# Performance work log

Hardware: AMD Instinct MI355X
Metric: run time of the kernel (lower is better)

Reference implementation:

```python
import jax, jax.numpy as jnp
import numpy as np

N = 20000      # nodes
E = 320000     # edges (before self-loops)
D = 128        # esm_embeds
H = 4          # n_heads (layer 1)
G = 256        # graphs in batch
SLOPE = 0.2    # GATConv default negative_slope


def setup_inputs() -> dict:
    key = jax.random.key(0)
    ks = jax.random.split(key, 16)
    x = jax.random.normal(ks[0], (N, D), jnp.float32)
    src = jax.random.randint(ks[1], (E,), 0, N)
    off = jax.random.randint(ks[2], (E,), 1, N)
    dst = (src + off) % N  # guaranteed no self-loops (PyG removes then re-adds them)
    edge_index = jnp.stack([src, dst]).astype(jnp.int64)
    batch = jnp.sort(jax.random.randint(ks[3], (N,), 0, G)).astype(jnp.int64)
    s = 0.05
    W1 = jax.random.normal(ks[4], (D, H * D), jnp.float32) * s
    a_src1 = jax.random.normal(ks[5], (1, H, D), jnp.float32) * s
    a_dst1 = jax.random.normal(ks[6], (1, H, D), jnp.float32) * s
    b1 = jnp.zeros((H * D,), jnp.float32)
    W2 = jax.random.normal(ks[7], (H * D, D), jnp.float32) * s
    a_src2 = jax.random.normal(ks[8], (1, 1, D), jnp.float32) * s
    a_dst2 = jax.random.normal(ks[9], (1, 1, D), jnp.float32) * s
    b2 = jnp.zeros((D,), jnp.float32)
    fc1_w = jax.random.normal(ks[10], (D, 16), jnp.float32) * s
    fc1_b = jnp.zeros((16,), jnp.float32)
    fc2_w = jax.random.normal(ks[11], (16, 1), jnp.float32) * s
    fc2_b = jnp.zeros((1,), jnp.float32)
    return {"x": x, "edge_index": edge_index, "batch": batch,
            "W1": W1, "a_src1": a_src1, "a_dst1": a_dst1, "b1": b1,
            "W2": W2, "a_src2": a_src2, "a_dst2": a_dst2, "b2": b2,
            "fc1_w": fc1_w, "fc1_b": fc1_b, "fc2_w": fc2_w, "fc2_b": fc2_b}


def _gat_conv(h, src, dst, a_src, a_dst, n):
    """h: [n, heads, C]; returns aggregated [n, heads, C] (PyG GATConv message passing)."""
    al_s = jnp.sum(h * a_src, axis=-1)  # [n, heads]
    al_d = jnp.sum(h * a_dst, axis=-1)  # [n, heads]
    e = jax.nn.leaky_relu(al_s[src] + al_d[dst], SLOPE)  # [Etot, heads]
    m = jax.lax.stop_gradient(jax.ops.segment_max(e, dst, num_segments=n))
    ex = jnp.exp(e - m[dst])
    denom = jax.ops.segment_sum(ex, dst, num_segments=n)
    alpha = ex / denom[dst]                               # per-destination softmax
    msg = h[src] * alpha[..., None]                       # [Etot, heads, C]
    return jax.ops.segment_sum(msg, dst, num_segments=n)


def reference(x, edge_index, batch, W1, a_src1, a_dst1, b1,
              W2, a_src2, a_dst2, b2, fc1_w, fc1_b, fc2_w, fc2_b):
    n = x.shape[0]
    loop = jnp.arange(n, dtype=edge_index.dtype)
    src = jnp.concatenate([edge_index[0], loop])  # GATConv add_self_loops=True
    dst = jnp.concatenate([edge_index[1], loop])
    # layer 1: heads=H, concat -> [n, H*D], then ELU (dropout is identity in eval)
    h1 = (x @ W1).reshape(n, H, D)
    o1 = _gat_conv(h1, src, dst, a_src1, a_dst1, n).reshape(n, H * D) + b1
    x1 = jax.nn.elu(o1)
    # layer 2: heads=1, concat -> [n, D], then ReLU
    h2 = (x1 @ W2).reshape(n, 1, D)
    o2 = _gat_conv(h2, src, dst, a_src2, a_dst2, n).reshape(n, D) + b2
    x2 = jax.nn.relu(o2)
    # global max pool over graphs; x2 >= 0 so clamping handles any empty segment
    pooled = jnp.maximum(jax.ops.segment_max(x2, batch, num_segments=G), 0.0)
    hfc = jax.nn.relu(pooled @ fc1_w + fc1_b)
    return hfc @ fc2_w + fc2_b  # [G, 1]
```

## Files before the change

kernel.cpp:

```cpp
#include <hip/hip_runtime.h>
#include <hip/hip_fp16.h>

#define N_NODES 20000
#define E_EDGES 320000
#define D_DIM   128
#define H1HEADS 4
#define G_GRAPHS 256
#define SLOPE   0.2f

typedef short short8 __attribute__((ext_vector_type(8)));
typedef float float4v __attribute__((ext_vector_type(4)));

__global__ void cnt_k(const int* __restrict__ dst, int* __restrict__ cnt) {
    int e = blockIdx.x * blockDim.x + threadIdx.x;
    if (e < E_EDGES) atomicAdd(&cnt[dst[e]], 1);
}

__global__ __launch_bounds__(256) void scan_k(const int* __restrict__ cnt,
                                              int* __restrict__ rowptr) {
    __shared__ int s[256];
    const int t = threadIdx.x;
    const int CH = (N_NODES + 255) / 256;
    int base = t * CH;
    int sum = 0;
    for (int i = 0; i < CH; ++i) {
        int idx = base + i;
        if (idx < N_NODES) sum += cnt[idx];
    }
    s[t] = sum;
    __syncthreads();
    for (int off = 1; off < 256; off <<= 1) {
        int v = (t >= off) ? s[t - off] : 0;
        __syncthreads();
        s[t] += v;
        __syncthreads();
    }
    int run = (t > 0) ? s[t - 1] : 0;
    for (int i = 0; i < CH; ++i) {
        int idx = base + i;
        if (idx < N_NODES) { rowptr[idx] = run; run += cnt[idx]; }
    }
    if (t == 255) rowptr[N_NODES] = run;
}

__global__ void scat_k(const int* __restrict__ src, const int* __restrict__ dst,
                       const int* __restrict__ rowptr, int* __restrict__ cur,
                       int* __restrict__ csrsrc) {
    int e = blockIdx.x * blockDim.x + threadIdx.x;
    if (e >= E_EDGES) return;
    int d = dst[e];
    int p = rowptr[d] + atomicAdd(&cur[d], 1);
    csrsrc[p] = src[e];
}

__device__ __forceinline__ unsigned short f2bf(float f) {
    unsigned u = __float_as_uint(f);
    unsigned r = u + 0x7FFFu + ((u >> 16) & 1u);
    return (unsigned short)(r >> 16);
}
__device__ __forceinline__ float bf2f(unsigned short b) {
    return __uint_as_float((unsigned)b << 16);
}

__global__ void split_k(const float* __restrict__ in, unsigned short* __restrict__ hi,
                        unsigned short* __restrict__ lo, const int n) {
    int i = blockIdx.x * blockDim.x + threadIdx.x;
    if (i >= n) return;
    float v = in[i];
    unsigned short h = f2bf(v);
    hi[i] = h;
    lo[i] = f2bf(v - bf2f(h));
}

__global__ void splitT_k(const float* __restrict__ w, unsigned short* __restrict__ hiT,
                         unsigned short* __restrict__ loT, const int K, const int N) {
    int i = blockIdx.x * blockDim.x + threadIdx.x;
    if (i >= K * N) return;
    int k = i / N, n = i - k * N;
    float v = w[i];
    unsigned short h = f2bf(v);
    hiT[n * K + k] = h;
    loT[n * K + k] = f2bf(v - bf2f(h));
}

__device__ __forceinline__ void store_val(__half* p, float v) { *p = __float2half(v); }
__device__ __forceinline__ void store_val(float* p, float v) { *p = v; }

template <typename OT>
__global__ __launch_bounds__(256) void mgemm_k(const unsigned short* __restrict__ Ahi,
                                               const unsigned short* __restrict__ Alo,
                                               const unsigned short* __restrict__ BThi,
                                               const unsigned short* __restrict__ BTlo,
                                               const int M, const int N, const int K,
                                               OT* __restrict__ C) {
    constexpr int SA = 72;
    __shared__ unsigned short Ah[64 * SA], Al[64 * SA];
    __shared__ unsigned short Bh[128 * SA], Bl[128 * SA];
    const int t = threadIdx.x;
    const int wave = t >> 6, lane = t & 63;
    const int q = lane >> 4, rr = lane & 15;
    const int row0 = blockIdx.x * 64;
    const int col0 = blockIdx.y * 128;
    const int wm = wave & 1, wn = wave >> 1;

    float4v acc[2][4];
#pragma unroll
    for (int i = 0; i < 2; ++i)
#pragma unroll
        for (int j = 0; j < 4; ++j) acc[i][j] = (float4v){0.f, 0.f, 0.f, 0.f};

    for (int kc = 0; kc < K; kc += 64) {
        __syncthreads();
#pragma unroll
        for (int i = 0; i < 2; ++i) {
            int u = t + i * 256;
            int m = u >> 3, mac = u & 7;
            int r = row0 + m;
            uint4 vh = {0, 0, 0, 0}, vl = {0, 0, 0, 0};
            if (r < M) {
                vh = *(const uint4*)(Ahi + (size_t)r * K + kc + mac * 8);
                vl = *(const uint4*)(Alo + (size_t)r * K + kc + mac * 8);
            }
            *(uint4*)(Ah + m * SA + mac * 8) = vh;
            *(uint4*)(Al + m * SA + mac * 8) = vl;
        }
#pragma unroll
        for (int i = 0; i < 4; ++i) {
            int u = t + i * 256;
            int n = u >> 3, mac = u & 7;
            *(uint4*)(Bh + n * SA + mac * 8) =
                *(const uint4*)(BThi + (size_t)(col0 + n) * K + kc + mac * 8);
            *(uint4*)(Bl + n * SA + mac * 8) =
                *(const uint4*)(BTlo + (size_t)(col0 + n) * K + kc + mac * 8);
        }
        __syncthreads();
#pragma unroll
        for (int ks = 0; ks < 2; ++ks) {
            const int ko = ks * 32 + q * 8;
            short8 ah[2], alo[2], bh[4], blo[4];
#pragma unroll
            for (int mt = 0; mt < 2; ++mt) {
                int m = (wm * 2 + mt) * 16 + rr;
                ah[mt]  = *(const short8*)(Ah + m * SA + ko);
                alo[mt] = *(const short8*)(Al + m * SA + ko);
            }
#pragma unroll
            for (int nt = 0; nt < 4; ++nt) {
                int n = (wn * 4 + nt) * 16 + rr;
                bh[nt]  = *(const short8*)(Bh + n * SA + ko);
                blo[nt] = *(const short8*)(Bl + n * SA + ko);
            }
#pragma unroll
            for (int mt = 0; mt < 2; ++mt)
#pragma unroll
                for (int nt = 0; nt < 4; ++nt) {
                    acc[mt][nt] = __builtin_amdgcn_mfma_f32_16x16x32_bf16(
                        ah[mt], bh[nt], acc[mt][nt], 0, 0, 0);
                    acc[mt][nt] = __builtin_amdgcn_mfma_f32_16x16x32_bf16(
                        ah[mt], blo[nt], acc[mt][nt], 0, 0, 0);
                    acc[mt][nt] = __builtin_amdgcn_mfma_f32_16x16x32_bf16(
                        alo[mt], bh[nt], acc[mt][nt], 0, 0, 0);
                }
        }
    }
#pragma unroll
    for (int mt = 0; mt < 2; ++mt) {
#pragma unroll
        for (int reg = 0; reg < 4; ++reg) {
            int r = row0 + (wm * 2 + mt) * 16 + q * 4 + reg;
            if (r < M) {
#pragma unroll
                for (int nt = 0; nt < 4; ++nt) {
                    int c = col0 + (wn * 4 + nt) * 16 + rr;
                    store_val(&C[(size_t)r * N + c], acc[mt][nt][reg]);
                }
            }
        }
    }
}

__device__ __forceinline__ int bitonic64(int key, int lane) {
#pragma unroll
    for (int k = 2; k <= 64; k <<= 1) {
#pragma unroll
        for (int j = k >> 1; j > 0; j >>= 1) {
            int other = __shfl_xor(key, j);
            bool up = ((lane & k) == 0);
            bool lower = ((lane & j) == 0);
            int mn = min(key, other), mx = max(key, other);
            key = (up == lower) ? mn : mx;
        }
    }
    return key;
}

__global__ __launch_bounds__(256) void al16_k(const __half* __restrict__ h,
                                              const float* __restrict__ a_src,
                                              const float* __restrict__ a_dst,
                                              float* __restrict__ als,
                                              float* __restrict__ ald,
                                              const int NH, const int H) {
    int wid = (blockIdx.x * blockDim.x + threadIdx.x) >> 6;
    int lane = threadIdx.x & 63;
    if (wid >= NH) return;
    int hh = wid % H;
    const __half2* row = (const __half2*)(h + (size_t)wid * 128);
    float2 v = __half22float2(row[lane]);
    float2 as2 = ((const float2*)(a_src + hh * 128))[lane];
    float2 ad2 = ((const float2*)(a_dst + hh * 128))[lane];
    float s = v.x * as2.x + v.y * as2.y;
    float d = v.x * ad2.x + v.y * ad2.y;
#pragma unroll
    for (int off = 32; off > 0; off >>= 1) {
        s += __shfl_down(s, off);
        d += __shfl_down(d, off);
    }
    if (lane == 0) { als[wid] = s; ald[wid] = d; }
}

__global__ __launch_bounds__(256) void al32_k(const float* __restrict__ h,
                                              const float* __restrict__ a_src,
                                              const float* __restrict__ a_dst,
                                              float* __restrict__ als,
                                              float* __restrict__ ald,
                                              const int NH) {
    int wid = (blockIdx.x * blockDim.x + threadIdx.x) >> 6;
    int lane = threadIdx.x & 63;
    if (wid >= NH) return;
    float2 v = ((const float2*)(h + (size_t)wid * 128))[lane];
    float2 as2 = ((const float2*)a_src)[lane];
    float2 ad2 = ((const float2*)a_dst)[lane];
    float s = v.x * as2.x + v.y * as2.y;
    float d = v.x * ad2.x + v.y * ad2.y;
#pragma unroll
    for (int off = 32; off > 0; off >>= 1) {
        s += __shfl_down(s, off);
        d += __shfl_down(d, off);
    }
    if (lane == 0) { als[wid] = s; ald[wid] = d; }
}

__device__ __forceinline__ float lrelu(float v) { return (v > 0.f) ? v : SLOPE * v; }

__global__ __launch_bounds__(256) void agg1_k(const __half* __restrict__ h,
                                              const float4* __restrict__ als4,
                                              const float4* __restrict__ ald4,
                                              const int* __restrict__ rowptr,
                                              const int* __restrict__ csrsrc,
                                              const float* __restrict__ bias,
                                              unsigned short* __restrict__ x1hi,
                                              unsigned short* __restrict__ x1lo) {
    const int node = (blockIdx.x * blockDim.x + threadIdx.x) >> 6;
    if (node >= N_NODES) return;
    const int lane = threadIdx.x & 63;
    const int head = lane >> 4;
    const int r0 = rowptr[node];
    const int deg = rowptr[node + 1] - r0;
    const int tot = deg + 1;
    const float4 aldn = ald4[node];

    float acc[8] = {};
    float4 d4;

    if (tot <= 64) {
        int key = 0x7FFFFFFF;
        if (lane < deg) key = csrsrc[r0 + lane];
        else if (lane == deg) key = node;
        key = bitonic64(key, lane);
        int s = (lane < tot) ? key : node;
        float4 l4 = make_float4(-1e30f, -1e30f, -1e30f, -1e30f);
        if (lane < tot) {
            float4 a = als4[s];
            l4.x = lrelu(a.x + aldn.x); l4.y = lrelu(a.y + aldn.y);
            l4.z = lrelu(a.z + aldn.z); l4.w = lrelu(a.w + aldn.w);
        }
        float4 m4 = l4;
#pragma unroll
        for (int off = 32; off > 0; off >>= 1) {
            m4.x = fmaxf(m4.x, __shfl_xor(m4.x, off));
            m4.y = fmaxf(m4.y, __shfl_xor(m4.y, off));
            m4.z = fmaxf(m4.z, __shfl_xor(m4.z, off));
            m4.w = fmaxf(m4.w, __shfl_xor(m4.w, off));
        }
        float4 w4 = make_float4(0.f, 0.f, 0.f, 0.f);
        if (lane < tot) {
            w4.x = expf(l4.x - m4.x); w4.y = expf(l4.y - m4.y);
            w4.z = expf(l4.z - m4.z); w4.w = expf(l4.w - m4.w);
        }
        d4 = w4;
#pragma unroll
        for (int off = 32; off > 0; off >>= 1) {
            d4.x += __shfl_xor(d4.x, off);
            d4.y += __shfl_xor(d4.y, off);
            d4.z += __shfl_xor(d4.z, off);
            d4.w += __shfl_xor(d4.w, off);
        }
        for (int j = 0; j < tot; ++j) {
            int sj = __shfl(s, j);
            float w0 = __shfl(w4.x, j), w1 = __shfl(w4.y, j);
            float w2 = __shfl(w4.z, j), w3 = __shfl(w4.w, j);
            float wj = (head < 2) ? (head == 0 ? w0 : w1) : (head == 2 ? w2 : w3);
            const uint4 pk = *((const uint4*)(h + (size_t)sj * 512) + lane);
            const __half2* p2 = (const __half2*)&pk;
            float2 f0 = __half22float2(p2[0]);
            float2 f1 = __half22float2(p2[1]);
            float2 f2 = __half22float2(p2[2]);
            float2 f3 = __half22float2(p2[3]);
            acc[0] += wj * f0.x; acc[1] += wj * f0.y;
            acc[2] += wj * f1.x; acc[3] += wj * f1.y;
            acc[4] += wj * f2.x; acc[5] += wj * f2.y;
            acc[6] += wj * f3.x; acc[7] += wj * f3.y;
        }
    } else {
        float4 m4 = make_float4(-1e30f, -1e30f, -1e30f, -1e30f);
        for (int base = 0; base < tot; base += 64) {
            int j = base + lane;
            float4 l4 = make_float4(-1e30f, -1e30f, -1e30f, -1e30f);
            if (j < tot) {
                int s = (j < deg) ? csrsrc[r0 + j] : node;
                float4 a = als4[s];
                l4.x = lrelu(a.x + aldn.x); l4.y = lrelu(a.y + aldn.y);
                l4.z = lrelu(a.z + aldn.z); l4.w = lrelu(a.w + aldn.w);
            }
#pragma unroll
            for (int off = 32; off > 0; off >>= 1) {
                l4.x = fmaxf(l4.x, __shfl_xor(l4.x, off));
                l4.y = fmaxf(l4.y, __shfl_xor(l4.y, off));
                l4.z = fmaxf(l4.z, __shfl_xor(l4.z, off));
                l4.w = fmaxf(l4.w, __shfl_xor(l4.w, off));
            }
            m4.x = fmaxf(m4.x, l4.x); m4.y = fmaxf(m4.y, l4.y);
            m4.z = fmaxf(m4.z, l4.z); m4.w = fmaxf(m4.w, l4.w);
        }
        d4 = make_float4(0.f, 0.f, 0.f, 0.f);
        for (int base = 0; base < tot; base += 64) {
            int j = base + lane;
            int s = node;
            float4 w4 = make_float4(0.f, 0.f, 0.f, 0.f);
            if (j < tot) {
                if (j < deg) s = csrsrc[r0 + j];
                float4 a = als4[s];
                w4.x = expf(lrelu(a.x + aldn.x) - m4.x);
                w4.y = expf(lrelu(a.y + aldn.y) - m4.y);
                w4.z = expf(lrelu(a.z + aldn.z) - m4.z);
                w4.w = expf(lrelu(a.w + aldn.w) - m4.w);
            }
            float4 p4 = w4;
#pragma unroll
            for (int off = 32; off > 0; off >>= 1) {
                p4.x += __shfl_xor(p4.x, off);
                p4.y += __shfl_xor(p4.y, off);
                p4.z += __shfl_xor(p4.z, off);
                p4.w += __shfl_xor(p4.w, off);
            }
            d4.x += p4.x; d4.y += p4.y; d4.z += p4.z; d4.w += p4.w;
            int lim = min(64, tot - base);
            for (int j2 = 0; j2 < lim; ++j2) {
                int sj = __shfl(s, j2);
                float w0 = __shfl(w4.x, j2), w1 = __shfl(w4.y, j2);
                float w2 = __shfl(w4.z, j2), w3 = __shfl(w4.w, j2);
                float wj = (head < 2) ? (head == 0 ? w0 : w1) : (head == 2 ? w2 : w3);
                const uint4 pk = *((const uint4*)(h + (size_t)sj * 512) + lane);
                const __half2* p2 = (const __half2*)&pk;
                float2 f0 = __half22float2(p2[0]);
                float2 f1 = __half22float2(p2[1]);
                float2 f2 = __half22float2(p2[2]);
                float2 f3 = __half22float2(p2[3]);
                acc[0] += wj * f0.x; acc[1] += wj * f0.y;
                acc[2] += wj * f1.x; acc[3] += wj * f1.y;
                acc[4] += wj * f2.x; acc[5] += wj * f2.y;
                acc[6] += wj * f3.x; acc[7] += wj * f3.y;
            }
        }
    }

    const float dsel = (head < 2) ? (head == 0 ? d4.x : d4.y) : (head == 2 ? d4.z : d4.w);
    const float inv = 1.f / dsel;
    const float4 b0 = ((const float4*)bias)[lane * 2];
    const float4 b1 = ((const float4*)bias)[lane * 2 + 1];
    float v[8];
    v[0] = acc[0] * inv + b0.x; v[1] = acc[1] * inv + b0.y;
    v[2] = acc[2] * inv + b0.z; v[3] = acc[3] * inv + b0.w;
    v[4] = acc[4] * inv + b1.x; v[5] = acc[5] * inv + b1.y;
    v[6] = acc[6] * inv + b1.z; v[7] = acc[7] * inv + b1.w;
    uint4 ph, pl;
    unsigned short* hps = (unsigned short*)&ph;
    unsigned short* lps = (unsigned short*)&pl;
#pragma unroll
    for (int k = 0; k < 8; ++k) {
        float e = (v[k] > 0.f) ? v[k] : expm1f(v[k]);
        unsigned short hb = f2bf(e);
        hps[k] = hb;
        lps[k] = f2bf(e - bf2f(hb));
    }
    *(uint4*)(x1hi + (size_t)node * 512 + lane * 8) = ph;
    *(uint4*)(x1lo + (size_t)node * 512 + lane * 8) = pl;
}

__global__ __launch_bounds__(256) void agg2_k(const float* __restrict__ h,
                                              const float* __restrict__ als,
                                              const float* __restrict__ ald,
                                              const int* __restrict__ rowptr,
                                              const int* __restrict__ csrsrc,
                                              const float* __restrict__ bias,
                                              const int* __restrict__ batch,
                                              int* __restrict__ pooled) {
    const int node = (blockIdx.x * blockDim.x + threadIdx.x) >> 6;
    if (node >= N_NODES) return;
    const int lane = threadIdx.x & 63;
    const int r0 = rowptr[node];
    const int deg = rowptr[node + 1] - r0;
    const int tot = deg + 1;
    const float aldn = ald[node];

    float acc0 = 0.f, acc1 = 0.f;
    float denom;

    if (tot <= 64) {
        int key = 0x7FFFFFFF;
        if (lane < deg) key = csrsrc[r0 + lane];
        else if (lane == deg) key = node;
        key = bitonic64(key, lane);
        int s = (lane < tot) ? key : node;
        float l = -1e30f, w = 0.f;
        if (lane < tot) l = lrelu(als[s] + aldn);
        float m = l;
#pragma unroll
        for (int off = 32; off > 0; off >>= 1) m = fmaxf(m, __shfl_xor(m, off));
        if (lane < tot) w = expf(l - m);
        denom = w;
#pragma unroll
        for (int off = 32; off > 0; off >>= 1) denom += __shfl_xor(denom, off);
        for (int j = 0; j < tot; ++j) {
            int sj = __shfl(s, j);
            float wj = __shfl(w, j);
            float2 f = ((const float2*)(h + (size_t)sj * 128))[lane];
            acc0 += wj * f.x;
            acc1 += wj * f.y;
        }
    } else {
        float m = -1e30f;
        for (int base = 0; base < tot; base += 64) {
            int j = base + lane;
            float l = -1e30f;
            if (j < tot) {
                int s = (j < deg) ? csrsrc[r0 + j] : node;
                l = lrelu(als[s] + aldn);
            }
#pragma unroll
            for (int off = 32; off > 0; off >>= 1) l = fmaxf(l, __shfl_xor(l, off));
            m = fmaxf(m, l);
        }
        denom = 0.f;
        for (int base = 0; base < tot; base += 64) {
            int j = base + lane;
            int s = node;
            float w = 0.f;
            if (j < tot) {
                if (j < deg) s = csrsrc[r0 + j];
                w = expf(lrelu(als[s] + aldn) - m);
            }
            float ws = w;
#pragma unroll
            for (int off = 32; off > 0; off >>= 1) ws += __shfl_xor(ws, off);
            denom += ws;
            int lim = min(64, tot - base);
            for (int j2 = 0; j2 < lim; ++j2) {
                int sj = __shfl(s, j2);
                float wj = __shfl(w, j2);
                float2 f = ((const float2*)(h + (size_t)sj * 128))[lane];
                acc0 += wj * f.x;
                acc1 += wj * f.y;
            }
        }
    }

    const float inv = 1.f / denom;
    float v0 = fmaxf(acc0 * inv + bias[lane * 2], 0.f);
    float v1 = fmaxf(acc1 * inv + bias[lane * 2 + 1], 0.f);
    int* pb = pooled + batch[node] * 128;
    atomicMax(&pb[lane * 2], __float_as_int(v0));
    atomicMax(&pb[lane * 2 + 1], __float_as_int(v1));
}

__global__ __launch_bounds__(64) void fc_k(const float* __restrict__ pooled,
                                           const float* __restrict__ w1,
                                           const float* __restrict__ b1,
                                           const float* __restrict__ w2,
                                           const float* __restrict__ b2,
                                           float* __restrict__ out) {
    int g = blockIdx.x;
    __shared__ float p[128];
    int t = threadIdx.x;
    p[t] = pooled[g * 128 + t];
    p[t + 64] = pooled[g * 128 + 64 + t];
    __syncthreads();
    float acc = 0.f;
    if (t < 16) {
        float s = b1[t];
        for (int c = 0; c < 128; ++c) s += p[c] * w1[c * 16 + t];
        s = fmaxf(s, 0.f);
        acc = s * w2[t];
    }
#pragma unroll
    for (int off = 8; off > 0; off >>= 1) acc += __shfl_down(acc, off);
    if (t == 0) out[g] = acc + b2[0];
}

extern "C" void kernel_launch(void* const* d_in, const int* in_sizes, int n_in,
                              void* d_out, int out_size, void* d_ws, size_t ws_size,
                              hipStream_t stream) {
    const float* x      = (const float*)d_in[0];
    const int*   ei     = (const int*)d_in[1];
    const int*   batch  = (const int*)d_in[2];
    const float* W1     = (const float*)d_in[3];
    const float* a_src1 = (const float*)d_in[4];
    const float* a_dst1 = (const float*)d_in[5];
    const float* b1     = (const float*)d_in[6];
    const float* W2     = (const float*)d_in[7];
    const float* a_src2 = (const float*)d_in[8];
    const float* a_dst2 = (const float*)d_in[9];
    const float* b2     = (const float*)d_in[10];
    const float* fc1w   = (const float*)d_in[11];
    const float* fc1b   = (const float*)d_in[12];
    const float* fc2w   = (const float*)d_in[13];
    const float* fc2b   = (const float*)d_in[14];
    float* out = (float*)d_out;

    const int* src = ei;
    const int* dst = ei + E_EDGES;

    int*   cnt    = (int*)d_ws;
    int*   cur    = cnt + 20000;
    int*   pooled = cur + 20000;
    int*   rowptr = pooled + 32768;
    int*   csrsrc = rowptr + 20004;
    __half* h1h   = (__half*)(csrsrc + 320000);
    float* h2     = (float*)(h1h + 10240000);
    float* als1   = h2 + 2560000;
    float* ald1   = als1 + 80000;
    float* als2   = ald1 + 80000;
    float* ald2   = als2 + 20000;
    unsigned short* xhi   = (unsigned short*)(ald2 + 20000);
    unsigned short* xlo   = xhi + 2560000;
    unsigned short* w1thi = xlo + 2560000;
    unsigned short* w1tlo = w1thi + 65536;
    unsigned short* w2thi = w1tlo + 65536;
    unsigned short* w2tlo = w2thi + 65536;
    unsigned short* x1hi  = w2tlo + 65536;
    unsigned short* x1lo  = x1hi + 10240000;

    (void)hipMemsetAsync(d_ws, 0, 72768 * 4, stream);

    cnt_k<<<(E_EDGES + 255) / 256, 256, 0, stream>>>(dst, cnt);
    scan_k<<<1, 256, 0, stream>>>(cnt, rowptr);
    scat_k<<<(E_EDGES + 255) / 256, 256, 0, stream>>>(src, dst, rowptr, cur, csrsrc);

    split_k<<<(N_NODES * 128 + 255) / 256, 256, 0, stream>>>(x, xhi, xlo, N_NODES * 128);
    splitT_k<<<(128 * 512 + 255) / 256, 256, 0, stream>>>(W1, w1thi, w1tlo, 128, 512);
    splitT_k<<<(512 * 128 + 255) / 256, 256, 0, stream>>>(W2, w2thi, w2tlo, 512, 128);

    mgemm_k<__half><<<dim3(313, 4), 256, 0, stream>>>(xhi, xlo, w1thi, w1tlo,
                                                      N_NODES, 512, 128, h1h);

    al16_k<<<(N_NODES * H1HEADS) / 4, 256, 0, stream>>>(h1h, a_src1, a_dst1, als1, ald1,
                                                        N_NODES * H1HEADS, H1HEADS);

    agg1_k<<<N_NODES / 4, 256, 0, stream>>>(h1h, (const float4*)als1, (const float4*)ald1,
                                            rowptr, csrsrc, b1, x1hi, x1lo);

    mgemm_k<float><<<dim3(313, 1), 256, 0, stream>>>(x1hi, x1lo, w2thi, w2tlo,
                                                     N_NODES, 128, 512, h2);

    al32_k<<<N_NODES / 4, 256, 0, stream>>>(h2, a_src2, a_dst2, als2, ald2, N_NODES);

    agg2_k<<<N_NODES / 4, 256, 0, stream>>>(h2, als2, ald2, rowptr, csrsrc, b2,
                                            batch, pooled);

    fc_k<<<G_GRAPHS, 64, 0, stream>>>((const float*)pooled, fc1w, fc1b, fc2w, fc2b, out);
}
```

Before: 336.9 us.

## Prefetch GEMM tiles, presort CSR once, fuse split kernels, store h2 in fp16

```diff
diff --git a/kernel.cpp b/kernel.cpp
--- a/kernel.cpp
+++ b/kernel.cpp
@@ -10,6 +10,7 @@
 
 typedef short short8 __attribute__((ext_vector_type(8)));
 typedef float float4v __attribute__((ext_vector_type(4)));
+typedef unsigned short us;
 
 __global__ void cnt_k(const int* __restrict__ dst, int* __restrict__ cnt) {
     int e = blockIdx.x * blockDim.x + threadIdx.x;
@@ -53,49 +54,85 @@
     csrsrc[p] = src[e];
 }
 
-__device__ __forceinline__ unsigned short f2bf(float f) {
+__device__ __forceinline__ int bitonic64(int key, int lane) {
+#pragma unroll
+    for (int k = 2; k <= 64; k <<= 1) {
+#pragma unroll
+        for (int j = k >> 1; j > 0; j >>= 1) {
+            int other = __shfl_xor(key, j);
+            bool up = ((lane & k) == 0);
+            bool lower = ((lane & j) == 0);
+            int mn = min(key, other), mx = max(key, other);
+            key = (up == lower) ? mn : mx;
+        }
+    }
+    return key;
+}
+
+__global__ __launch_bounds__(256) void sortb_k(const int* __restrict__ rowptr,
+                                               int* __restrict__ csrsrc) {
+    const int node = (blockIdx.x * blockDim.x + threadIdx.x) >> 6;
+    if (node >= N_NODES) return;
+    const int lane = threadIdx.x & 63;
+    const int r0 = rowptr[node];
+    const int deg = rowptr[node + 1] - r0;
+    if (deg <= 1 || deg > 64) return;
+    int key = 0x7FFFFFFF;
+    if (lane < deg) key = csrsrc[r0 + lane];
+    key = bitonic64(key, lane);
+    if (lane < deg) csrsrc[r0 + lane] = key;
+}
+
+__device__ __forceinline__ us f2bf(float f) {
     unsigned u = __float_as_uint(f);
     unsigned r = u + 0x7FFFu + ((u >> 16) & 1u);
-    return (unsigned short)(r >> 16);
-}
-__device__ __forceinline__ float bf2f(unsigned short b) {
+    return (us)(r >> 16);
+}
+__device__ __forceinline__ float bf2f(us b) {
     return __uint_as_float((unsigned)b << 16);
 }
 
-__global__ void split_k(const float* __restrict__ in, unsigned short* __restrict__ hi,
-                        unsigned short* __restrict__ lo, const int n) {
+__global__ void splitall_k(const float* __restrict__ x, us* __restrict__ xhi,
+                           us* __restrict__ xlo,
+                           const float* __restrict__ W1, us* __restrict__ w1thi,
+                           us* __restrict__ w1tlo,
+                           const float* __restrict__ W2, us* __restrict__ w2thi,
+                           us* __restrict__ w2tlo) {
     int i = blockIdx.x * blockDim.x + threadIdx.x;
-    if (i >= n) return;
-    float v = in[i];
-    unsigned short h = f2bf(v);
-    hi[i] = h;
-    lo[i] = f2bf(v - bf2f(h));
-}
-
-__global__ void splitT_k(const float* __restrict__ w, unsigned short* __restrict__ hiT,
-                         unsigned short* __restrict__ loT, const int K, const int N) {
-    int i = blockIdx.x * blockDim.x + threadIdx.x;
-    if (i >= K * N) return;
-    int k = i / N, n = i - k * N;
-    float v = w[i];
-    unsigned short h = f2bf(v);
-    hiT[n * K + k] = h;
-    loT[n * K + k] = f2bf(v - bf2f(h));
+    if (i < N_NODES * 128) {
+        float v = x[i];
+        us h = f2bf(v);
+        xhi[i] = h; xlo[i] = f2bf(v - bf2f(h));
+    }
+    if (i < 128 * 512) {
+        {
+            int k = i >> 9, n = i & 511;
+            float v = W1[i];
+            us h = f2bf(v);
+            w1thi[n * 128 + k] = h; w1tlo[n * 128 + k] = f2bf(v - bf2f(h));
+        }
+        {
+            int k = i >> 7, n = i & 127;
+            float v = W2[i];
+            us h = f2bf(v);
+            w2thi[n * 512 + k] = h; w2tlo[n * 512 + k] = f2bf(v - bf2f(h));
+        }
+    }
 }
 
 __device__ __forceinline__ void store_val(__half* p, float v) { *p = __float2half(v); }
 __device__ __forceinline__ void store_val(float* p, float v) { *p = v; }
 
 template <typename OT>
-__global__ __launch_bounds__(256) void mgemm_k(const unsigned short* __restrict__ Ahi,
-                                               const unsigned short* __restrict__ Alo,
-                                               const unsigned short* __restrict__ BThi,
-                                               const unsigned short* __restrict__ BTlo,
+__global__ __launch_bounds__(256) void mgemm_k(const us* __restrict__ Ahi,
+                                               const us* __restrict__ Alo,
+                                               const us* __restrict__ BThi,
+                                               const us* __restrict__ BTlo,
                                                const int M, const int N, const int K,
                                                OT* __restrict__ C) {
     constexpr int SA = 72;
-    __shared__ unsigned short Ah[64 * SA], Al[64 * SA];
-    __shared__ unsigned short Bh[128 * SA], Bl[128 * SA];
+    __shared__ us Ah[64 * SA], Al[64 * SA];
+    __shared__ us Bh[128 * SA], Bl[128 * SA];
     const int t = threadIdx.x;
     const int wave = t >> 6, lane = t & 63;
     const int q = lane >> 4, rr = lane & 15;
@@ -103,37 +140,59 @@
     const int col0 = blockIdx.y * 128;
     const int wm = wave & 1, wn = wave >> 1;
 
-    float4v acc[2][4];
-#pragma unroll
-    for (int i = 0; i < 2; ++i)
-#pragma unroll
-        for (int j = 0; j < 4; ++j) acc[i][j] = (float4v){0.f, 0.f, 0.f, 0.f};
-
-    for (int kc = 0; kc < K; kc += 64) {
-        __syncthreads();
+    uint4 ra[2][2], rb[4][2];
+
+    auto load_chunk = [&](int kc) {
 #pragma unroll
         for (int i = 0; i < 2; ++i) {
             int u = t + i * 256;
             int m = u >> 3, mac = u & 7;
             int r = row0 + m;
-            uint4 vh = {0, 0, 0, 0}, vl = {0, 0, 0, 0};
             if (r < M) {
-                vh = *(const uint4*)(Ahi + (size_t)r * K + kc + mac * 8);
-                vl = *(const uint4*)(Alo + (size_t)r * K + kc + mac * 8);
-            }
-            *(uint4*)(Ah + m * SA + mac * 8) = vh;
-            *(uint4*)(Al + m * SA + mac * 8) = vl;
+                ra[i][0] = *(const uint4*)(Ahi + (size_t)r * K + kc + mac * 8);
+                ra[i][1] = *(const uint4*)(Alo + (size_t)r * K + kc + mac * 8);
+            } else {
+                ra[i][0] = make_uint4(0, 0, 0, 0);
+                ra[i][1] = make_uint4(0, 0, 0, 0);
+            }
         }
 #pragma unroll
         for (int i = 0; i < 4; ++i) {
             int u = t + i * 256;
             int n = u >> 3, mac = u & 7;
-            *(uint4*)(Bh + n * SA + mac * 8) =
-                *(const uint4*)(BThi + (size_t)(col0 + n) * K + kc + mac * 8);
-            *(uint4*)(Bl + n * SA + mac * 8) =
-                *(const uint4*)(BTlo + (size_t)(col0 + n) * K + kc + mac * 8);
-        }
+            rb[i][0] = *(const uint4*)(BThi + (size_t)(col0 + n) * K + kc + mac * 8);
+            rb[i][1] = *(const uint4*)(BTlo + (size_t)(col0 + n) * K + kc + mac * 8);
+        }
+    };
+    auto write_lds = [&]() {
+#pragma unroll
+        for (int i = 0; i < 2; ++i) {
+            int u = t + i * 256;
+            int m = u >> 3, mac = u & 7;
+            *(uint4*)(Ah + m * SA + mac * 8) = ra[i][0];
+            *(uint4*)(Al + m * SA + mac * 8) = ra[i][1];
+        }
+#pragma unroll
+        for (int i = 0; i < 4; ++i) {
+            int u = t + i * 256;
+            int n = u >> 3, mac = u & 7;
+            *(uint4*)(Bh + n * SA + mac * 8) = rb[i][0];
+            *(uint4*)(Bl + n * SA + mac * 8) = rb[i][1];
+        }
+    };
+
+    float4v acc[2][4];
+#pragma unroll
+    for (int i = 0; i < 2; ++i)
+#pragma unroll
+        for (int j = 0; j < 4; ++j) acc[i][j] = (float4v){0.f, 0.f, 0.f, 0.f};
+
+    load_chunk(0);
+    for (int kc = 0; kc < K; kc += 64) {
         __syncthreads();
+        write_lds();
+        __syncthreads();
+        if (kc + 64 < K) load_chunk(kc + 64);
 #pragma unroll
         for (int ks = 0; ks < 2; ++ks) {
             const int ko = ks * 32 + q * 8;
@@ -177,21 +236,6 @@
             }
         }
     }
-}
-
-__device__ __forceinline__ int bitonic64(int key, int lane) {
-#pragma unroll
-    for (int k = 2; k <= 64; k <<= 1) {
-#pragma unroll
-        for (int j = k >> 1; j > 0; j >>= 1) {
-            int other = __shfl_xor(key, j);
-            bool up = ((lane & k) == 0);
-            bool lower = ((lane & j) == 0);
-            int mn = min(key, other), mx = max(key, other);
-            key = (up == lower) ? mn : mx;
-        }
-    }
-    return key;
 }
 
 __global__ __launch_bounds__(256) void al16_k(const __half* __restrict__ h,
@@ -218,28 +262,6 @@
     if (lane == 0) { als[wid] = s; ald[wid] = d; }
 }
 
-__global__ __launch_bounds__(256) void al32_k(const float* __restrict__ h,
-                                              const float* __restrict__ a_src,
-                                              const float* __restrict__ a_dst,
-                                              float* __restrict__ als,
-                                              float* __restrict__ ald,
-                                              const int NH) {
-    int wid = (blockIdx.x * blockDim.x + threadIdx.x) >> 6;
-    int lane = threadIdx.x & 63;
-    if (wid >= NH) return;
-    float2 v = ((const float2*)(h + (size_t)wid * 128))[lane];
-    float2 as2 = ((const float2*)a_src)[lane];
-    float2 ad2 = ((const float2*)a_dst)[lane];
-    float s = v.x * as2.x + v.y * as2.y;
-    float d = v.x * ad2.x + v.y * ad2.y;
-#pragma unroll
-    for (int off = 32; off > 0; off >>= 1) {
-        s += __shfl_down(s, off);
-        d += __shfl_down(d, off);
-    }
-    if (lane == 0) { als[wid] = s; ald[wid] = d; }
-}
-
 __device__ __forceinline__ float lrelu(float v) { return (v > 0.f) ? v : SLOPE * v; }
 
 __global__ __launch_bounds__(256) void agg1_k(const __half* __restrict__ h,
@@ -248,11 +270,14 @@
                                               const int* __restrict__ rowptr,
                                               const int* __restrict__ csrsrc,
                                               const float* __restrict__ bias,
-                                              unsigned short* __restrict__ x1hi,
-                                              unsigned short* __restrict__ x1lo) {
+                                              us* __restrict__ x1hi,
+                                              us* __restrict__ x1lo) {
+    __shared__ int   ss[4][64];
+    __shared__ float ws[4][64][4];
     const int node = (blockIdx.x * blockDim.x + threadIdx.x) >> 6;
     if (node >= N_NODES) return;
     const int lane = threadIdx.x & 63;
+    const int wv = threadIdx.x >> 6;
     const int head = lane >> 4;
     const int r0 = rowptr[node];
     const int deg = rowptr[node + 1] - r0;
@@ -263,11 +288,8 @@
     float4 d4;
 
     if (tot <= 64) {
-        int key = 0x7FFFFFFF;
-        if (lane < deg) key = csrsrc[r0 + lane];
-        else if (lane == deg) key = node;
-        key = bitonic64(key, lane);
-        int s = (lane < tot) ? key : node;
+        int s = node;
+        if (lane < deg) s = csrsrc[r0 + lane];
         float4 l4 = make_float4(-1e30f, -1e30f, -1e30f, -1e30f);
         if (lane < tot) {
             float4 a = als4[s];
@@ -295,11 +317,11 @@
             d4.z += __shfl_xor(d4.z, off);
             d4.w += __shfl_xor(d4.w, off);
         }
+        ss[wv][lane] = s;
+        *(float4*)&ws[wv][lane][0] = w4;
         for (int j = 0; j < tot; ++j) {
-            int sj = __shfl(s, j);
-            float w0 = __shfl(w4.x, j), w1 = __shfl(w4.y, j);
-            float w2 = __shfl(w4.z, j), w3 = __shfl(w4.w, j);
-            float wj = (head < 2) ? (head == 0 ? w0 : w1) : (head == 2 ? w2 : w3);
+            int sj = ss[wv][j];
+            float wj = ws[wv][j][head];
             const uint4 pk = *((const uint4*)(h + (size_t)sj * 512) + lane);
             const __half2* p2 = (const __half2*)&pk;
             float2 f0 = __half22float2(p2[0]);
@@ -384,12 +406,12 @@
     v[4] = acc[4] * inv + b1.x; v[5] = acc[5] * inv + b1.y;
     v[6] = acc[6] * inv + b1.z; v[7] = acc[7] * inv + b1.w;
     uint4 ph, pl;
-    unsigned short* hps = (unsigned short*)&ph;
-    unsigned short* lps = (unsigned short*)&pl;
+    us* hps = (us*)&ph;
+    us* lps = (us*)&pl;
 #pragma unroll
     for (int k = 0; k < 8; ++k) {
         float e = (v[k] > 0.f) ? v[k] : expm1f(v[k]);
-        unsigned short hb = f2bf(e);
+        us hb = f2bf(e);
         hps[k] = hb;
         lps[k] = f2bf(e - bf2f(hb));
     }
@@ -397,7 +419,7 @@
     *(uint4*)(x1lo + (size_t)node * 512 + lane * 8) = pl;
 }
 
-__global__ __launch_bounds__(256) void agg2_k(const float* __restrict__ h,
+__global__ __launch_bounds__(256) void agg2_k(const __half* __restrict__ h,
                                               const float* __restrict__ als,
                                               const float* __restrict__ ald,
                                               const int* __restrict__ rowptr,
@@ -405,9 +427,12 @@
                                               const float* __restrict__ bias,
                                               const int* __restrict__ batch,
                                               int* __restrict__ pooled) {
+    __shared__ int   ss[4][64];
+    __shared__ float ws[4][64];
     const int node = (blockIdx.x * blockDim.x + threadIdx.x) >> 6;
     if (node >= N_NODES) return;
     const int lane = threadIdx.x & 63;
+    const int wv = threadIdx.x >> 6;
     const int r0 = rowptr[node];
     const int deg = rowptr[node + 1] - r0;
     const int tot = deg + 1;
@@ -417,11 +442,8 @@
     float denom;
 
     if (tot <= 64) {
-        int key = 0x7FFFFFFF;
-        if (lane < deg) key = csrsrc[r0 + lane];
-        else if (lane == deg) key = node;
-        key = bitonic64(key, lane);
-        int s = (lane < tot) ? key : node;
+        int s = node;
+        if (lane < deg) s = csrsrc[r0 + lane];
         float l = -1e30f, w = 0.f;
         if (lane < tot) l = lrelu(als[s] + aldn);
         float m = l;
@@ -431,10 +453,12 @@
         denom = w;
 #pragma unroll
         for (int off = 32; off > 0; off >>= 1) denom += __shfl_xor(denom, off);
+        ss[wv][lane] = s;
+        ws[wv][lane] = w;
         for (int j = 0; j < tot; ++j) {
-            int sj = __shfl(s, j);
-            float wj = __shfl(w, j);
-            float2 f = ((const float2*)(h + (size_t)sj * 128))[lane];
+            int sj = ss[wv][j];
+            float wj = ws[wv][j];
+            float2 f = __half22float2(((const __half2*)(h + (size_t)sj * 128))[lane]);
             acc0 += wj * f.x;
             acc1 += wj * f.y;
         }
@@ -460,15 +484,15 @@
                 if (j < deg) s = csrsrc[r0 + j];
                 w = expf(lrelu(als[s] + aldn) - m);
             }
-            float ws = w;
-#pragma unroll
-            for (int off = 32; off > 0; off >>= 1) ws += __shfl_xor(ws, off);
-            denom += ws;
+            float ws2 = w;
+#pragma unroll
+            for (int off = 32; off > 0; off >>= 1) ws2 += __shfl_xor(ws2, off);
+            denom += ws2;
             int lim = min(64, tot - base);
             for (int j2 = 0; j2 < lim; ++j2) {
                 int sj = __shfl(s, j2);
                 float wj = __shfl(w, j2);
-                float2 f = ((const float2*)(h + (size_t)sj * 128))[lane];
+                float2 f = __half22float2(((const __half2*)(h + (size_t)sj * 128))[lane]);
                 acc0 += wj * f.x;
                 acc1 += wj * f.y;
             }
@@ -536,29 +560,29 @@
     int*   rowptr = pooled + 32768;
     int*   csrsrc = rowptr + 20004;
     __half* h1h   = (__half*)(csrsrc + 320000);
-    float* h2     = (float*)(h1h + 10240000);
-    float* als1   = h2 + 2560000;
+    __half* h2h   = h1h + 10240000;
+    float* als1   = (float*)(h2h + 2560000);
     float* ald1   = als1 + 80000;
     float* als2   = ald1 + 80000;
     float* ald2   = als2 + 20000;
-    unsigned short* xhi   = (unsigned short*)(ald2 + 20000);
-    unsigned short* xlo   = xhi + 2560000;
-    unsigned short* w1thi = xlo + 2560000;
-    unsigned short* w1tlo = w1thi + 65536;
-    unsigned short* w2thi = w1tlo + 65536;
-    unsigned short* w2tlo = w2thi + 65536;
-    unsigned short* x1hi  = w2tlo + 65536;
-    unsigned short* x1lo  = x1hi + 10240000;
+    us* xhi   = (us*)(ald2 + 20000);
+    us* xlo   = xhi + 2560000;
+    us* w1thi = xlo + 2560000;
+    us* w1tlo = w1thi + 65536;
+    us* w2thi = w1tlo + 65536;
+    us* w2tlo = w2thi + 65536;
+    us* x1hi  = w2tlo + 65536;
+    us* x1lo  = x1hi + 10240000;
 
     (void)hipMemsetAsync(d_ws, 0, 72768 * 4, stream);
 
     cnt_k<<<(E_EDGES + 255) / 256, 256, 0, stream>>>(dst, cnt);
     scan_k<<<1, 256, 0, stream>>>(cnt, rowptr);
     scat_k<<<(E_EDGES + 255) / 256, 256, 0, stream>>>(src, dst, rowptr, cur, csrsrc);
-
-    split_k<<<(N_NODES * 128 + 255) / 256, 256, 0, stream>>>(x, xhi, xlo, N_NODES * 128);
-    splitT_k<<<(128 * 512 + 255) / 256, 256, 0, stream>>>(W1, w1thi, w1tlo, 128, 512);
-    splitT_k<<<(512 * 128 + 255) / 256, 256, 0, stream>>>(W2, w2thi, w2tlo, 512, 128);
+    sortb_k<<<N_NODES / 4, 256, 0, stream>>>(rowptr, csrsrc);
+
+    splitall_k<<<(N_NODES * 128 + 255) / 256, 256, 0, stream>>>(
+        x, xhi, xlo, W1, w1thi, w1tlo, W2, w2thi, w2tlo);
 
     mgemm_k<__half><<<dim3(313, 4), 256, 0, stream>>>(xhi, xlo, w1thi, w1tlo,
                                                       N_NODES, 512, 128, h1h);
@@ -569,12 +593,12 @@
     agg1_k<<<N_NODES / 4, 256, 0, stream>>>(h1h, (const float4*)als1, (const float4*)ald1,
                                             rowptr, csrsrc, b1, x1hi, x1lo);
 
-    mgemm_k<float><<<dim3(313, 1), 256, 0, stream>>>(x1hi, x1lo, w2thi, w2tlo,
-                                                     N_NODES, 128, 512, h2);
-
-    al32_k<<<N_NODES / 4, 256, 0, stream>>>(h2, a_src2, a_dst2, als2, ald2, N_NODES);
-
-    agg2_k<<<N_NODES / 4, 256, 0, stream>>>(h2, als2, ald2, rowptr, csrsrc, b2,
+    mgemm_k<__half><<<dim3(313, 1), 256, 0, stream>>>(x1hi, x1lo, w2thi, w2tlo,
+                                                      N_NODES, 128, 512, h2h);
+
+    al16_k<<<N_NODES / 4, 256, 0, stream>>>(h2h, a_src2, a_dst2, als2, ald2, N_NODES, 1);
+
+    agg2_k<<<N_NODES / 4, 256, 0, stream>>>(h2h, als2, ald2, rowptr, csrsrc, b2,
                                             batch, pooled);
 
     fc_k<<<G_GRAPHS, 64, 0, stream>>>((const float*)pooled, fc1w, fc1b, fc2w, fc2b, out);
```

After: 367.2 us. 1.09x slower.
